# Performance work log

Measured on AMD Instinct MI355X. Metric: run time of the kernel, lower is better.

The kernel has to match this reference:

```python
import jax, jax.numpy as jnp
import numpy as np

C = 80          # NUM_CLASSES
D = 8525        # total anchors over FPN levels (640 input: 80^2+40^2+20^2+10^2+5^2)
B = 64
EPS = 1e-6


def setup_inputs() -> dict:
    key = jax.random.key(0)
    ks = jax.random.split(key, 8)
    outs = jax.random.normal(ks[0], (B, D, C + 5), dtype=jnp.float32)
    grids = jax.random.uniform(ks[1], (D, 2), dtype=jnp.float32) * 640.0  # anchor centers (px)
    # --- build gres = [gcls(C), centerness(1), g_ltrb(4), mask_pp(1), mask_pos(1), pad(1)] ---
    labels = jax.random.randint(ks[2], (B, D), 0, C)
    mask_pos = (jax.random.uniform(ks[3], (B, D)) < 0.10).astype(jnp.float32)  # in-box positives
    mask_pp = (jax.random.uniform(ks[4], (B, D)) < 0.05).astype(jnp.float32)   # center-radius positives
    gcls = jax.nn.one_hot(labels, C, dtype=jnp.float32) * mask_pos[..., None]
    gcenterness = jax.random.uniform(ks[5], (B, D), dtype=jnp.float32)
    off = jax.random.uniform(ks[6], (B, D, 4), dtype=jnp.float32) * 64.0 + 1.0
    gx = grids[None, :, 0]
    gy = grids[None, :, 1]
    g_ltrb = jnp.stack([gx - off[..., 0], gy - off[..., 1],
                        gx + off[..., 2], gy + off[..., 3]], axis=-1)
    gres = jnp.concatenate([gcls,
                            gcenterness[..., None],
                            g_ltrb,
                            mask_pp[..., None],
                            mask_pos[..., None],
                            jnp.zeros((B, D, 1), jnp.float32)], axis=-1)  # [B, D, 88]
    nums_pos = jax.random.randint(ks[7], (B,), 1, 21).astype(jnp.int32)
    return {"outs": outs, "gres": gres, "grids": grids, "nums_pos": nums_pos}


def _giou(p, g):
    # elementwise GIoU on ltrb boxes, p/g: [..., 4]
    ix1 = jnp.maximum(p[..., 0], g[..., 0]); iy1 = jnp.maximum(p[..., 1], g[..., 1])
    ix2 = jnp.minimum(p[..., 2], g[..., 2]); iy2 = jnp.minimum(p[..., 3], g[..., 3])
    inter = jnp.clip(ix2 - ix1, 0.0) * jnp.clip(iy2 - iy1, 0.0)
    area_p = jnp.clip(p[..., 2] - p[..., 0], 0.0) * jnp.clip(p[..., 3] - p[..., 1], 0.0)
    area_g = jnp.clip(g[..., 2] - g[..., 0], 0.0) * jnp.clip(g[..., 3] - g[..., 1], 0.0)
    union = area_p + area_g - inter
    iou = inter / (union + EPS)
    cx1 = jnp.minimum(p[..., 0], g[..., 0]); cy1 = jnp.minimum(p[..., 1], g[..., 1])
    cx2 = jnp.maximum(p[..., 2], g[..., 2]); cy2 = jnp.maximum(p[..., 3], g[..., 3])
    c_area = (cx2 - cx1) * (cy2 - cy1)
    return iou - (c_area - union) / (c_area + EPS)


def reference(outs, gres, grids, nums_pos):
    np_f = nums_pos.astype(jnp.float32)
    # ---- cls: focal loss over all anchors ----
    pcls = jax.nn.sigmoid(outs[..., :C])          # [B, D, C]
    gcls = gres[..., :C]
    pos_m = (gcls == 1.0).astype(pcls.dtype)
    l_pos = -0.25 * (1.0 - pcls) ** 2 * jnp.log(pcls + EPS) * pos_m
    l_neg = -0.75 * pcls ** 2 * jnp.log(1.0 - pcls + EPS) * (1.0 - pos_m)
    l_cls_pos = jnp.mean(jnp.sum(l_pos, axis=(1, 2)) / np_f)
    l_cls_neg = jnp.mean(jnp.sum(l_neg, axis=(1, 2)) / np_f)
    # ---- conf: BCE(pconf, 1) over center-radius positives ----
    mask_pp = (gres[..., C + 5] == 1.0).astype(outs.dtype)
    pconf = jax.nn.sigmoid(outs[..., C])
    bce = -jnp.log(pconf + EPS)                    # target = ones
    l_conf = 5.0 * jnp.mean(jnp.sum(bce * mask_pp, axis=-1) / np_f)
    # ---- reg: masked GIoU over in-box positives ----
    mask_pos = (gres[..., C + 6] == 1.0).astype(outs.dtype)
    poff = outs[..., C + 1:C + 5]
    gxy = grids[None]                              # [1, D, 2]
    pboxes = jnp.concatenate([gxy - poff[..., :2], gxy + poff[..., 2:]], axis=-1)
    g_ltrb = gres[..., C + 1:C + 5]
    giou = _giou(pboxes, g_ltrb)                   # [B, D]
    gcenter = gres[..., C]
    n_pos = jnp.maximum(jnp.sum(mask_pos), 1.0)
    l_reg = 5.0 * jnp.sum((1.0 - giou) * gcenter * mask_pos) / n_pos
    return l_cls_pos + l_cls_neg + l_conf + l_reg
```

## Files before the change

### kernel.cpp

```cpp
#include <hip/hip_runtime.h>

namespace {

constexpr int   kC    = 80;
constexpr int   kD    = 8525;
constexpr int   kB    = 64;
constexpr float kEps  = 1e-6f;
constexpr int   kOC   = 85;
constexpr int   kGC   = 88;
constexpr int   kBlk  = 256;
constexpr int   kPB   = kD * kOC;
constexpr int   kKpb  = 32;
constexpr int   kNA   = kB * kKpb;
constexpr int   kChunk = (kPB + kKpb - 1) / kKpb;
constexpr int   kNB   = 768;
constexpr int   kNT   = kNA + kNB;

__device__ __forceinline__ float wave_reduce(float v) {
#pragma unroll
  for (int o = 32; o > 0; o >>= 1) v += __shfl_down(v, o, 64);
  return v;
}

__device__ __forceinline__ float sigmoidf(float x) {
  return 1.0f / (1.0f + __expf(-x));
}

__global__ __launch_bounds__(kBlk) void floss_fused(
    const float* __restrict__ outs, const float* __restrict__ gres,
    const float* __restrict__ grids, const int* __restrict__ nums_pos,
    float* __restrict__ partials) {
  const int bid = blockIdx.x;
  const int tid = threadIdx.x;
  float pm = 0.f, pr = 0.f, pn = 0.f;

  if (bid < kNB) {
    const int nrow = kB * kD;
    for (int row = bid * kBlk + tid; row < nrow; row += kNB * kBlk) {
      const int b = row / kD;
      const int d = row - b * kD;
      const size_t gbase = (size_t)row * kGC;
      const float4 t0 = *(const float4*)(gres + gbase + 80);
      const float4 t1 = *(const float4*)(gres + gbase + 84);
      const float scale = 1.0f / (64.0f * (float)nums_pos[b]);
      if (t1.y == 1.0f) {
        const float pc = sigmoidf(outs[(size_t)row * kOC + kC]);
        pm += -5.0f * __logf(pc + kEps) * scale;
      }
      if (t1.z == 1.0f) {
        pn += 1.0f;
        int lab = 0;
        const float4* gc = (const float4*)(gres + gbase);
#pragma unroll 5
        for (int j = 0; j < 20; ++j) {
          const float4 v = gc[j];
          if (v.x == 1.0f) lab = 4 * j;
          if (v.y == 1.0f) lab = 4 * j + 1;
          if (v.z == 1.0f) lab = 4 * j + 2;
          if (v.w == 1.0f) lab = 4 * j + 3;
        }
        const float x = outs[(size_t)row * kOC + lab];
        const float p = sigmoidf(x);
        const float om = 1.0f - p;
        const float lp = -0.25f * om * om * __logf(p + kEps);
        const float ln = -0.75f * p * p * __logf(om + kEps);
        pm += (lp - ln) * scale;
        const float gx = grids[2 * d + 0];
        const float gy = grids[2 * d + 1];
        const float* po = outs + (size_t)row * kOC + kC + 1;
        const float p0 = gx - po[0], p1 = gy - po[1];
        const float p2 = gx + po[2], p3 = gy + po[3];
        const float g0 = t0.y, g1 = t0.z, g2 = t0.w, g3 = t1.x;
        const float iw = fmaxf(fminf(p2, g2) - fmaxf(p0, g0), 0.f);
        const float ih = fmaxf(fminf(p3, g3) - fmaxf(p1, g1), 0.f);
        const float inter = iw * ih;
        const float ap = fmaxf(p2 - p0, 0.f) * fmaxf(p3 - p1, 0.f);
        const float ag = fmaxf(g2 - g0, 0.f) * fmaxf(g3 - g1, 0.f);
        const float un = ap + ag - inter;
        const float iou = inter / (un + kEps);
        const float ca = (fmaxf(p2, g2) - fminf(p0, g0)) *
                         (fmaxf(p3, g3) - fminf(p1, g1));
        const float giou = iou - (ca - un) / (ca + kEps);
        pr += (1.0f - giou) * t0.x;
      }
    }
  } else {
    const int sb = bid - kNB;
    const int b  = sb >> 5;
    const int k  = sb & 31;
    const long base = (long)b * kPB;
    const int  s = k * kChunk;
    const int  e = (s + kChunk < kPB) ? s + kChunk : kPB;
    const long gs = base + s;
    const long ge = base + e;
    const long gv = (gs + 3) & ~3L;
    const long gvend = gv + (((ge - gv) >> 2) << 2);
    float acc = 0.f;

    const int headc = (int)(gv - gs);
    if (tid < headc) {
      const long g = gs + tid;
      const unsigned c = (unsigned)(g - base) % 85u;
      if (c < 80u) {
        const float p = sigmoidf(outs[g]);
        acc += p * p * __logf(1.0f - p + kEps);
      }
    }
    const int tailc = (int)(ge - gvend);
    if (tid < tailc) {
      const long g = gvend + tid;
      const unsigned c = (unsigned)(g - base) % 85u;
      if (c < 80u) {
        const float p = sigmoidf(outs[g]);
        acc += p * p * __logf(1.0f - p + kEps);
      }
    }

    const int nvec = (int)((gvend - gv) >> 2);
    for (int v = tid; v < nvec; v += kBlk) {
      const long g = gv + 4L * v;
      const float4 val = *(const float4*)(outs + g);
      unsigned c = (unsigned)(g - base) % 85u;
      if (c < 80u) { const float p = sigmoidf(val.x); acc += p * p * __logf(1.0f - p + kEps); }
      c = (c + 1 >= 85u) ? 0u : c + 1;
      if (c < 80u) { const float p = sigmoidf(val.y); acc += p * p * __logf(1.0f - p + kEps); }
      c = (c + 1 >= 85u) ? 0u : c + 1;
      if (c < 80u) { const float p = sigmoidf(val.z); acc += p * p * __logf(1.0f - p + kEps); }
      c = (c + 1 >= 85u) ? 0u : c + 1;
      if (c < 80u) { const float p = sigmoidf(val.w); acc += p * p * __logf(1.0f - p + kEps); }
    }
    const float scale = 1.0f / (64.0f * (float)nums_pos[b]);
    pm = -0.75f * acc * scale;
  }

  __shared__ float sm[3][kBlk / 64];
  const float vm = wave_reduce(pm);
  const float vr = wave_reduce(pr);
  const float vn = wave_reduce(pn);
  const int lane = tid & 63;
  const int w    = tid >> 6;
  if (lane == 0) { sm[0][w] = vm; sm[1][w] = vr; sm[2][w] = vn; }
  __syncthreads();
  if (tid == 0) {
    float m = 0.f, r = 0.f, n = 0.f;
#pragma unroll
    for (int j = 0; j < kBlk / 64; ++j) { m += sm[0][j]; r += sm[1][j]; n += sm[2][j]; }
    partials[bid * 3 + 0] = m;
    partials[bid * 3 + 1] = r;
    partials[bid * 3 + 2] = n;
  }
}

__global__ __launch_bounds__(kBlk) void floss_final(
    const float* __restrict__ partials, float* __restrict__ out) {
  float m = 0.f, r = 0.f, n = 0.f;
  for (int i = threadIdx.x; i < kNT; i += kBlk) {
    m += partials[i * 3 + 0];
    r += partials[i * 3 + 1];
    n += partials[i * 3 + 2];
  }
  __shared__ float sm[3][kBlk / 64];
  m = wave_reduce(m); r = wave_reduce(r); n = wave_reduce(n);
  const int lane = threadIdx.x & 63;
  const int w    = threadIdx.x >> 6;
  if (lane == 0) { sm[0][w] = m; sm[1][w] = r; sm[2][w] = n; }
  __syncthreads();
  if (threadIdx.x == 0) {
    float tm = 0.f, tr = 0.f, tn = 0.f;
#pragma unroll
    for (int j = 0; j < kBlk / 64; ++j) { tm += sm[0][j]; tr += sm[1][j]; tn += sm[2][j]; }
    out[0] = tm + 5.0f * tr / fmaxf(tn, 1.0f);
  }
}

}

extern "C" void kernel_launch(void* const* d_in, const int* in_sizes, int n_in,
                              void* d_out, int out_size, void* d_ws, size_t ws_size,
                              hipStream_t stream) {
  const float* outs     = (const float*)d_in[0];
  const float* gres     = (const float*)d_in[1];
  const float* grids    = (const float*)d_in[2];
  const int*   nums_pos = (const int*)d_in[3];
  float* partials = (float*)d_ws;

  floss_fused<<<kNT, kBlk, 0, stream>>>(outs, gres, grids, nums_pos, partials);
  floss_final<<<1, kBlk, 0, stream>>>(partials, (float*)d_out);
}
```

Measured before the change: 70.83 us.

## Merge dense and row loss paths into one block grid, drop per-element modulo

Removes the separate per-row block range and has each block handle a contiguous slice of anchors for one batch. The dense negative-loss sum now runs over every element of the slice, including the five non-class columns, with no modulo-85 class check, and then subtracts the terms for columns 80-84 in the per-row pass. Those columns are reused for the confidence and box terms. Division is replaced with the hardware reciprocal intrinsic. This cuts index arithmetic and branches and avoids reading the outs rows twice, at the cost of some extra transcendental work on the five extra columns and small numerical differences from the add-then-subtract.

Result: faster. 67.06 us (-5.3%).

```diff
diff --git a/kernel.cpp b/kernel.cpp
--- a/kernel.cpp
+++ b/kernel.cpp
@@ -10,11 +10,9 @@
 constexpr int   kGC   = 88;
 constexpr int   kBlk  = 256;
 constexpr int   kPB   = kD * kOC;
-constexpr int   kKpb  = 32;
-constexpr int   kNA   = kB * kKpb;
-constexpr int   kChunk = (kPB + kKpb - 1) / kKpb;
-constexpr int   kNB   = 768;
-constexpr int   kNT   = kNA + kNB;
+constexpr int   kSpb  = 32;
+constexpr int   kRPS  = (kD + kSpb - 1) / kSpb;
+constexpr int   kNT   = kB * kSpb;
 
 __device__ __forceinline__ float wave_reduce(float v) {
 #pragma unroll
@@ -22,8 +20,14 @@
   return v;
 }
 
-__device__ __forceinline__ float sigmoidf(float x) {
-  return 1.0f / (1.0f + __expf(-x));
+__device__ __forceinline__ float fast_rcp(float x) {
+  return __builtin_amdgcn_rcpf(x);
+}
+
+__device__ __forceinline__ float lneg_raw(float x) {
+  const float t = __expf(-x);
+  const float p = fast_rcp(1.0f + t);
+  return p * p * __logf(1.0f - p + kEps);
 }
 
 __global__ __launch_bounds__(kBlk) void floss_fused(
@@ -32,105 +36,87 @@
     float* __restrict__ partials) {
   const int bid = blockIdx.x;
   const int tid = threadIdx.x;
+  const int b   = bid >> 5;
+  const int sb  = bid & 31;
+  const int r0  = sb * kRPS;
+  const int r1  = (r0 + kRPS < kD) ? r0 + kRPS : kD;
+  const float scale = fast_rcp(64.0f * (float)nums_pos[b]);
+
   float pm = 0.f, pr = 0.f, pn = 0.f;
 
-  if (bid < kNB) {
-    const int nrow = kB * kD;
-    for (int row = bid * kBlk + tid; row < nrow; row += kNB * kBlk) {
-      const int b = row / kD;
-      const int d = row - b * kD;
-      const size_t gbase = (size_t)row * kGC;
-      const float4 t0 = *(const float4*)(gres + gbase + 80);
-      const float4 t1 = *(const float4*)(gres + gbase + 84);
-      const float scale = 1.0f / (64.0f * (float)nums_pos[b]);
-      if (t1.y == 1.0f) {
-        const float pc = sigmoidf(outs[(size_t)row * kOC + kC]);
-        pm += -5.0f * __logf(pc + kEps) * scale;
+  {
+    const int gA = b * kPB + r0 * kOC;
+    const int gB = b * kPB + r1 * kOC;
+    const int gv = (gA + 3) & ~3;
+    const int nvec = (gB - gv) >> 2;
+    const int gvend = gv + (nvec << 2);
+    float a0 = 0.f, a1 = 0.f, a2 = 0.f, a3 = 0.f;
+    if (tid < gv - gA)    a0 += lneg_raw(outs[gA + tid]);
+    if (tid < gB - gvend) a1 += lneg_raw(outs[gvend + tid]);
+#pragma unroll 2
+    for (int v = tid; v < nvec; v += kBlk) {
+      const float4 x = *(const float4*)(outs + gv + 4 * v);
+      a0 += lneg_raw(x.x);
+      a1 += lneg_raw(x.y);
+      a2 += lneg_raw(x.z);
+      a3 += lneg_raw(x.w);
+    }
+    pm += -0.75f * scale * ((a0 + a1) + (a2 + a3));
+  }
+
+  for (int r = r0 + tid; r < r1; r += kBlk) {
+    const int row = b * kD + r;
+    const float* orow = outs + (size_t)row * kOC;
+    const float x80 = orow[80], x81 = orow[81], x82 = orow[82],
+                x83 = orow[83], x84 = orow[84];
+    const float t5 = ((lneg_raw(x80) + lneg_raw(x81)) +
+                      (lneg_raw(x82) + lneg_raw(x83))) + lneg_raw(x84);
+    pm += 0.75f * scale * t5;
+
+    const size_t gbase = (size_t)row * kGC;
+    const float4 t0 = *(const float4*)(gres + gbase + 80);
+    const float4 t1 = *(const float4*)(gres + gbase + 84);
+
+    if (t1.y == 1.0f) {
+      const float pc = fast_rcp(1.0f + __expf(-x80));
+      pm += -5.0f * __logf(pc + kEps) * scale;
+    }
+    if (t1.z == 1.0f) {
+      pn += 1.0f;
+      int lab = 0;
+      const float4* gc = (const float4*)(gres + gbase);
+#pragma unroll 5
+      for (int j = 0; j < 20; ++j) {
+        const float4 v = gc[j];
+        if (v.x == 1.0f) lab = 4 * j;
+        if (v.y == 1.0f) lab = 4 * j + 1;
+        if (v.z == 1.0f) lab = 4 * j + 2;
+        if (v.w == 1.0f) lab = 4 * j + 3;
       }
-      if (t1.z == 1.0f) {
-        pn += 1.0f;
-        int lab = 0;
-        const float4* gc = (const float4*)(gres + gbase);
-#pragma unroll 5
-        for (int j = 0; j < 20; ++j) {
-          const float4 v = gc[j];
-          if (v.x == 1.0f) lab = 4 * j;
-          if (v.y == 1.0f) lab = 4 * j + 1;
-          if (v.z == 1.0f) lab = 4 * j + 2;
-          if (v.w == 1.0f) lab = 4 * j + 3;
-        }
-        const float x = outs[(size_t)row * kOC + lab];
-        const float p = sigmoidf(x);
-        const float om = 1.0f - p;
-        const float lp = -0.25f * om * om * __logf(p + kEps);
-        const float ln = -0.75f * p * p * __logf(om + kEps);
-        pm += (lp - ln) * scale;
-        const float gx = grids[2 * d + 0];
-        const float gy = grids[2 * d + 1];
-        const float* po = outs + (size_t)row * kOC + kC + 1;
-        const float p0 = gx - po[0], p1 = gy - po[1];
-        const float p2 = gx + po[2], p3 = gy + po[3];
-        const float g0 = t0.y, g1 = t0.z, g2 = t0.w, g3 = t1.x;
-        const float iw = fmaxf(fminf(p2, g2) - fmaxf(p0, g0), 0.f);
-        const float ih = fmaxf(fminf(p3, g3) - fmaxf(p1, g1), 0.f);
-        const float inter = iw * ih;
-        const float ap = fmaxf(p2 - p0, 0.f) * fmaxf(p3 - p1, 0.f);
-        const float ag = fmaxf(g2 - g0, 0.f) * fmaxf(g3 - g1, 0.f);
-        const float un = ap + ag - inter;
-        const float iou = inter / (un + kEps);
-        const float ca = (fmaxf(p2, g2) - fminf(p0, g0)) *
-                         (fmaxf(p3, g3) - fminf(p1, g1));
-        const float giou = iou - (ca - un) / (ca + kEps);
-        pr += (1.0f - giou) * t0.x;
-      }
+      const float x = orow[lab];
+      const float t = __expf(-x);
+      const float p = fast_rcp(1.0f + t);
+      const float om = 1.0f - p;
+      const float lp = -0.25f * om * om * __logf(p + kEps);
+      const float ln = -0.75f * p * p * __logf(om + kEps);
+      pm += (lp - ln) * scale;
+      const float gx = grids[2 * r + 0];
+      const float gy = grids[2 * r + 1];
+      const float p0 = gx - x81, p1 = gy - x82;
+      const float p2 = gx + x83, p3 = gy + x84;
+      const float g0 = t0.y, g1 = t0.z, g2 = t0.w, g3 = t1.x;
+      const float iw = fmaxf(fminf(p2, g2) - fmaxf(p0, g0), 0.f);
+      const float ih = fmaxf(fminf(p3, g3) - fmaxf(p1, g1), 0.f);
+      const float inter = iw * ih;
+      const float ap = fmaxf(p2 - p0, 0.f) * fmaxf(p3 - p1, 0.f);
+      const float ag = fmaxf(g2 - g0, 0.f) * fmaxf(g3 - g1, 0.f);
+      const float un = ap + ag - inter;
+      const float iou = inter * fast_rcp(un + kEps);
+      const float ca = (fmaxf(p2, g2) - fminf(p0, g0)) *
+                       (fmaxf(p3, g3) - fminf(p1, g1));
+      const float giou = iou - (ca - un) * fast_rcp(ca + kEps);
+      pr += (1.0f - giou) * t0.x;
     }
-  } else {
-    const int sb = bid - kNB;
-    const int b  = sb >> 5;
-    const int k  = sb & 31;
-    const long base = (long)b * kPB;
-    const int  s = k * kChunk;
-    const int  e = (s + kChunk < kPB) ? s + kChunk : kPB;
-    const long gs = base + s;
-    const long ge = base + e;
-    const long gv = (gs + 3) & ~3L;
-    const long gvend = gv + (((ge - gv) >> 2) << 2);
-    float acc = 0.f;
-
-    const int headc = (int)(gv - gs);
-    if (tid < headc) {
-      const long g = gs + tid;
-      const unsigned c = (unsigned)(g - base) % 85u;
-      if (c < 80u) {
-        const float p = sigmoidf(outs[g]);
-        acc += p * p * __logf(1.0f - p + kEps);
-      }
-    }
-    const int tailc = (int)(ge - gvend);
-    if (tid < tailc) {
-      const long g = gvend + tid;
-      const unsigned c = (unsigned)(g - base) % 85u;
-      if (c < 80u) {
-        const float p = sigmoidf(outs[g]);
-        acc += p * p * __logf(1.0f - p + kEps);
-      }
-    }
-
-    const int nvec = (int)((gvend - gv) >> 2);
-    for (int v = tid; v < nvec; v += kBlk) {
-      const long g = gv + 4L * v;
-      const float4 val = *(const float4*)(outs + g);
-      unsigned c = (unsigned)(g - base) % 85u;
-      if (c < 80u) { const float p = sigmoidf(val.x); acc += p * p * __logf(1.0f - p + kEps); }
-      c = (c + 1 >= 85u) ? 0u : c + 1;
-      if (c < 80u) { const float p = sigmoidf(val.y); acc += p * p * __logf(1.0f - p + kEps); }
-      c = (c + 1 >= 85u) ? 0u : c + 1;
-      if (c < 80u) { const float p = sigmoidf(val.z); acc += p * p * __logf(1.0f - p + kEps); }
-      c = (c + 1 >= 85u) ? 0u : c + 1;
-      if (c < 80u) { const float p = sigmoidf(val.w); acc += p * p * __logf(1.0f - p + kEps); }
-    }
-    const float scale = 1.0f / (64.0f * (float)nums_pos[b]);
-    pm = -0.75f * acc * scale;
   }
 
   __shared__ float sm[3][kBlk / 64];
```
